# Optimization experiments

Hardware: AMD Instinct MI355X
Metric: run time of the kernel (lower is better)

The kernel has to match this reference:

```python
import jax, jax.numpy as jnp
import numpy as np

B, N, T, H = 64, 15, 256, 128
TEMP = 1.0


def setup_inputs() -> dict:
    key = jax.random.key(0)
    ks = jax.random.split(key, 5)
    node_output = jax.random.normal(ks[0], (B, T, H), jnp.float32)
    neigh_output = jax.random.normal(ks[1], (B, N, T, H), jnp.float32)
    # causal-style mask: True = masked (t' > t); guarantees no fully-masked row
    attn_mask = jnp.broadcast_to(jnp.triu(jnp.ones((T, T), bool), k=1), (B, T, T))
    xav = (2.0 / (H + H)) ** 0.5  # xavier_normal std for square HxH
    Wq = jax.random.normal(ks[2], (H, H), jnp.float32) * xav
    Wk = jax.random.normal(ks[3], (H, H), jnp.float32) * xav
    Wv = jax.random.normal(ks[4], (H, H), jnp.float32) * xav
    z = jnp.zeros((H,), jnp.float32)  # biases init to 0 in init_params
    return dict(node_output=node_output, neigh_output=neigh_output,
                neighbors_number=N, attn_mask=attn_mask,
                Wq=Wq, bq=z, Wk=Wk, bk=z, Wv=Wv, bv=z)


def reference(node_output, neigh_output, neighbors_number, attn_mask,
              Wq, bq, Wk, bk, Wv, bv):
    b, t, h = node_output.shape
    n = neigh_output.shape[1]
    # key/value sequence: self node followed by its n neighbors -> [B, N+1, T, H]
    kv = jnp.concatenate([node_output[:, None], neigh_output], axis=1)
    # Linear (torch convention y = x W^T + b); query repeat collapses to single proj
    q = node_output @ Wq.T + bq                      # [B, T, H]
    k = kv @ Wk.T + bk                               # [B, N+1, T, H]
    v = kv.reshape(b, (n + 1) * t, h) @ Wv.T + bv    # [B, (N+1)*T, H]
    # scores: each query attends separately to every (source, timestep) key
    S = jnp.einsum('bth,bnsh->bnts', q, k)           # [B, N+1, T, T]
    # S_norm computed on the PRE-mask scores (original norms S.data before fill)
    S_norm = jnp.linalg.norm(S.reshape(b, -1), axis=-1)  # [B]
    S = jnp.where(attn_mask[:, None, :, :], -jnp.inf, S)
    S = jnp.transpose(S, (0, 2, 1, 3)) / TEMP        # [B, T, N+1, T]
    # joint softmax over all (N+1)*T keys at once
    A = jax.nn.softmax(S.reshape(b, t, (n + 1) * t), axis=-1)
    out = jnp.einsum('btk,bkh->bth', A, v)           # [B, T, H]
    return out, A.reshape(b, t, n + 1, t), S_norm
```

## Files before the change

kernel.cpp:

```cpp
#include <hip/hip_runtime.h>
#include <math.h>


constexpr int BB   = 64;
constexpr int TT   = 256;
constexpr int HH   = 128;
constexpr int KEYS = 4096;
constexpr int LDK  = 136;
constexpr int LDV  = 72;
constexpr int LDX  = 130;

typedef __attribute__((ext_vector_type(8)))  __bf16 bf16x8;
typedef __attribute__((ext_vector_type(16))) float  f32x16;

union BF8 { unsigned u[4]; bf16x8 v; };

__device__ __forceinline__ float4 ld4(const float* p) {
  return *reinterpret_cast<const float4*>(p);
}
__device__ __forceinline__ unsigned short f2bf(float x) {
  unsigned u = __float_as_uint(x);
  return (unsigned short)((u + 0x7fffu + ((u >> 16) & 1u)) >> 16);
}
__device__ __forceinline__ float bf2f(unsigned short h) {
  return __uint_as_float(((unsigned)h) << 16);
}
__device__ __forceinline__ unsigned packhl(float x) {
  unsigned short hi = f2bf(x);
  unsigned short lo = f2bf(x - bf2f(hi));
  return (unsigned)hi | (((unsigned)lo) << 16);
}
__device__ __forceinline__ void split2(float f0, float f1,
                                       unsigned& hw, unsigned& lw) {
  unsigned short h0 = f2bf(f0), h1 = f2bf(f1);
  unsigned short l0 = f2bf(f0 - bf2f(h0)), l1 = f2bf(f1 - bf2f(h1));
  hw = (unsigned)h0 | (((unsigned)h1) << 16);
  lw = (unsigned)l0 | (((unsigned)l1) << 16);
}
__device__ __forceinline__ void unpack8(const unsigned* p,
                                        bf16x8& hi, bf16x8& lo) {
  uint4 a = *reinterpret_cast<const uint4*>(p);
  uint4 c = *reinterpret_cast<const uint4*>(p + 4);
  BF8 H, L;
  H.u[0] = (a.x & 0xffffu) | (a.y << 16);
  H.u[1] = (a.z & 0xffffu) | (a.w << 16);
  H.u[2] = (c.x & 0xffffu) | (c.y << 16);
  H.u[3] = (c.z & 0xffffu) | (c.w << 16);
  L.u[0] = (a.x >> 16) | (a.y & 0xffff0000u);
  L.u[1] = (a.z >> 16) | (a.w & 0xffff0000u);
  L.u[2] = (c.x >> 16) | (c.y & 0xffff0000u);
  L.u[3] = (c.z >> 16) | (c.w & 0xffff0000u);
  hi = H.v; lo = L.v;
}
__device__ __forceinline__ f32x16 zero16() {
  f32x16 z;
  #pragma unroll
  for (int i = 0; i < 16; ++i) z[i] = 0.f;
  return z;
}
__device__ __forceinline__ f32x16 mfma3(bf16x8 ahi, bf16x8 alo,
                                        bf16x8 bhi, bf16x8 blo, f32x16 c) {
  c = __builtin_amdgcn_mfma_f32_32x32x16_bf16(ahi, bhi, c, 0, 0, 0);
  c = __builtin_amdgcn_mfma_f32_32x32x16_bf16(ahi, blo, c, 0, 0, 0);
  c = __builtin_amdgcn_mfma_f32_32x32x16_bf16(alo, bhi, c, 0, 0, 0);
  return c;
}

template<bool DOV>
__global__ __launch_bounds__(256, 2) void proj_mfma_kernel(
    const float* __restrict__ node, const float* __restrict__ neigh,
    const float* __restrict__ Wk_, const float* __restrict__ bk_,
    const float* __restrict__ Wv_, const float* __restrict__ bv_,
    unsigned* __restrict__ khl, unsigned short* __restrict__ v_t, int mode)
{
  __shared__ unsigned xp[128 * LDX];
  const int tid = threadIdx.x;
  const long r0 = (long)blockIdx.x * 128;

  #pragma unroll
  for (int i = 0; i < 16; ++i) {
    int slot = tid + 256 * i;
    int row = slot >> 5, h0 = (slot & 31) << 2;
    long r = r0 + row;
    const float* src;
    if (mode == 0) {
      src = node + r * HH;
    } else {
      long bb = r >> 12;
      int  n  = (int)((r >> 8) & 15);
      int  t  = (int)(r & 255);
      src = (n == 0) ? (node + (bb * TT + t) * HH)
                     : (neigh + ((bb * 15 + (n - 1)) * (long)TT + t) * HH);
    }
    float4 xv = ld4(src + h0);
    uint4 u;
    u.x = packhl(xv.x); u.y = packhl(xv.y);
    u.z = packhl(xv.z); u.w = packhl(xv.w);
    *reinterpret_cast<uint4*>(&xp[row * LDX + h0]) = u;
  }
  __syncthreads();

  const int l = tid & 63, w = tid >> 6, g = l >> 5, lane31 = l & 31;
  const int j = 32 * w + lane31;

  f32x16 accK[4];
  #pragma unroll
  for (int kt = 0; kt < 4; ++kt) accK[kt] = zero16();
  f32x16 accV[4];
  if constexpr (DOV) {
    #pragma unroll
    for (int kt = 0; kt < 4; ++kt) accV[kt] = zero16();
  }

  #pragma unroll
  for (int hs = 0; hs < 8; ++hs) {
    const int ho = 16 * hs + 8 * g;
    float4 wa = ld4(Wk_ + j * HH + ho), wb = ld4(Wk_ + j * HH + ho + 4);
    BF8 WH, WL;
    split2(wa.x, wa.y, WH.u[0], WL.u[0]);
    split2(wa.z, wa.w, WH.u[1], WL.u[1]);
    split2(wb.x, wb.y, WH.u[2], WL.u[2]);
    split2(wb.z, wb.w, WH.u[3], WL.u[3]);
    bf16x8 xhi[4], xlo[4];
    #pragma unroll
    for (int rt = 0; rt < 4; ++rt)
      unpack8(&xp[(32 * rt + lane31) * LDX + ho], xhi[rt], xlo[rt]);
    #pragma unroll
    for (int rt = 0; rt < 4; ++rt)
      accK[rt] = mfma3(xhi[rt], xlo[rt], WH.v, WL.v, accK[rt]);
    if constexpr (DOV) {
      float4 va = ld4(Wv_ + j * HH + ho), vb = ld4(Wv_ + j * HH + ho + 4);
      BF8 VH, VL;
      split2(va.x, va.y, VH.u[0], VL.u[0]);
      split2(va.z, va.w, VH.u[1], VL.u[1]);
      split2(vb.x, vb.y, VH.u[2], VL.u[2]);
      split2(vb.z, vb.w, VH.u[3], VL.u[3]);
      #pragma unroll
      for (int rt = 0; rt < 4; ++rt)
        accV[rt] = mfma3(VH.v, VL.v, xhi[rt], xlo[rt], accV[rt]);
    }
  }

  const float bK = bk_[j];
  #pragma unroll
  for (int kt = 0; kt < 4; ++kt) {
    #pragma unroll
    for (int reg = 0; reg < 16; ++reg) {
      int rm = (reg & 3) + 8 * (reg >> 2) + 4 * g;
      long r = r0 + 32 * kt + rm;
      khl[r * HH + j] = packhl(accK[kt][reg] + bK);
    }
  }
  if constexpr (DOV) {
    const int bidx = (int)(r0 >> 12);
    const int key0 = (int)(r0 & (KEYS - 1));
    float bvr[16];
    #pragma unroll
    for (int reg = 0; reg < 16; ++reg)
      bvr[reg] = bv_[32 * w + (reg & 3) + 8 * (reg >> 2) + 4 * g];
    #pragma unroll
    for (int kt = 0; kt < 4; ++kt) {
      #pragma unroll
      for (int reg = 0; reg < 16; ++reg) {
        int rm = (reg & 3) + 8 * (reg >> 2) + 4 * g;
        int jrow = 32 * w + rm;
        v_t[((long)(bidx * HH + jrow)) * KEYS + key0 + 32 * kt + lane31] =
            f2bf(accV[kt][reg] + bvr[reg]);
      }
    }
  }
}

__device__ __forceinline__ void load_qfrags(const unsigned* qp, int g,
                                            bf16x8 qhi[8], bf16x8 qlo[8])
{
  #pragma unroll
  for (int hs = 0; hs < 8; ++hs)
    unpack8(qp + 16 * hs + 8 * g, qhi[hs], qlo[hs]);
}

__global__ __launch_bounds__(128, 2) void passA_kernel(
    const unsigned* __restrict__ qhl, const unsigned* __restrict__ khl,
    float* __restrict__ m_part, float* __restrict__ l_part,
    float* __restrict__ ssq_part)
{
  __shared__ unsigned short Khi[64 * LDK];
  __shared__ unsigned short Klo[64 * LDK];
  const int tid = threadIdx.x, l = tid & 63, w = tid >> 6;
  const int g = (l >> 5) & 1, lane31 = l & 31;
  const int bx = blockIdx.x, b = bx >> 4, tq = (bx >> 2) & 3, ks = bx & 3;
  const int t0 = tq * 64;

  bf16x8 qhi[8], qlo[8];
  {
    const int t = t0 + 32 * w + lane31;
    load_qfrags(qhl + ((long)(b * TT + t)) * HH, g, qhi, qlo);
  }

  float mreg[16], lreg[16], ssq = 0.f;
  #pragma unroll
  for (int r = 0; r < 16; ++r) { mreg[r] = -1e30f; lreg[r] = 0.f; }

  for (int kt = 0; kt < 16; ++kt) {
    const int kb = ks * 1024 + kt * 64;
    __syncthreads();
    #pragma unroll
    for (int i = 0; i < 16; ++i) {
      int slot = i * 128 + tid;
      int row = slot >> 5, h0 = (slot & 31) << 2;
      uint4 a = *reinterpret_cast<const uint4*>(
          khl + ((long)(b * KEYS + kb + row)) * HH + h0);
      unsigned h01 = (a.x & 0xffffu) | (a.y << 16);
      unsigned h23 = (a.z & 0xffffu) | (a.w << 16);
      unsigned l01 = (a.x >> 16) | (a.y & 0xffff0000u);
      unsigned l23 = (a.z >> 16) | (a.w & 0xffff0000u);
      *reinterpret_cast<uint2*>(&Khi[row * LDK + h0]) = make_uint2(h01, h23);
      *reinterpret_cast<uint2*>(&Klo[row * LDK + h0]) = make_uint2(l01, l23);
    }
    __syncthreads();

    f32x16 acc0 = zero16(), acc1 = zero16();
    #pragma unroll
    for (int hs = 0; hs < 8; ++hs) {
      const int ho = 16 * hs + 8 * g;
      bf16x8 kh0 = *reinterpret_cast<const bf16x8*>(&Khi[lane31 * LDK + ho]);
      bf16x8 kl0 = *reinterpret_cast<const bf16x8*>(&Klo[lane31 * LDK + ho]);
      bf16x8 kh1 = *reinterpret_cast<const bf16x8*>(&Khi[(32 + lane31) * LDK + ho]);
      bf16x8 kl1 = *reinterpret_cast<const bf16x8*>(&Klo[(32 + lane31) * LDK + ho]);
      acc0 = mfma3(qhi[hs], qlo[hs], kh0, kl0, acc0);
      acc1 = mfma3(qhi[hs], qlo[hs], kh1, kl1, acc1);
    }

    const int st0 = (kb + lane31) & 255;
    const int st1 = (kb + 32 + lane31) & 255;
    #pragma unroll
    for (int reg = 0; reg < 16; ++reg) {
      const int tr = t0 + 32 * w + (reg & 3) + 8 * (reg >> 2) + 4 * g;
      float s0 = acc0[reg], s1 = acc1[reg];
      ssq = fmaf(s0, s0, fmaf(s1, s1, ssq));
      bool msk0 = st0 > tr, msk1 = st1 > tr;
      float v0 = msk0 ? -1e30f : s0;
      float v1 = msk1 ? -1e30f : s1;
      float mn = fmaxf(mreg[reg], fmaxf(v0, v1));
      float sc = __expf(mreg[reg] - mn);
      float p0 = msk0 ? 0.f : __expf(s0 - mn);
      float p1 = msk1 ? 0.f : __expf(s1 - mn);
      lreg[reg] = fmaf(lreg[reg], sc, p0 + p1);
      mreg[reg] = mn;
    }
  }

  #pragma unroll
  for (int reg = 0; reg < 16; ++reg) {
    #pragma unroll
    for (int off = 1; off < 32; off <<= 1) {
      float mo = __shfl_xor(mreg[reg], off);
      float lo = __shfl_xor(lreg[reg], off);
      float mn = fmaxf(mreg[reg], mo);
      lreg[reg] = lreg[reg] * __expf(mreg[reg] - mn) + lo * __expf(mo - mn);
      mreg[reg] = mn;
    }
  }
  if (lane31 == 0) {
    #pragma unroll
    for (int reg = 0; reg < 16; ++reg) {
      const int tr = t0 + 32 * w + (reg & 3) + 8 * (reg >> 2) + 4 * g;
      m_part[ks * (BB * TT) + b * TT + tr] = mreg[reg];
      l_part[ks * (BB * TT) + b * TT + tr] = lreg[reg];
    }
  }
  #pragma unroll
  for (int off = 1; off < 64; off <<= 1) ssq += __shfl_xor(ssq, off);
  __syncthreads();
  float* red = reinterpret_cast<float*>(Khi);
  if (l == 0) red[w] = ssq;
  __syncthreads();
  if (tid == 0) ssq_part[bx] = red[0] + red[1];
}

__global__ void merge_ml_kernel(const float* __restrict__ m_part,
                                const float* __restrict__ l_part,
                                float* __restrict__ m_ws,
                                float* __restrict__ l_ws)
{
  int idx = blockIdx.x * 256 + threadIdx.x;
  if (idx >= BB * TT) return;
  float m = -1e30f;
  #pragma unroll
  for (int k = 0; k < 4; ++k) m = fmaxf(m, m_part[k * (BB * TT) + idx]);
  float lsum = 0.f;
  #pragma unroll
  for (int k = 0; k < 4; ++k)
    lsum += l_part[k * (BB * TT) + idx] * __expf(m_part[k * (BB * TT) + idx] - m);
  m_ws[idx] = m;
  l_ws[idx] = lsum;
}

__global__ __launch_bounds__(256, 2) void passB_kernel(
    const unsigned* __restrict__ qhl, const unsigned* __restrict__ khl,
    const unsigned short* __restrict__ v_t,
    const float* __restrict__ m_ws, const float* __restrict__ l_ws,
    float* __restrict__ A_out, float* __restrict__ opart)
{
  __shared__ unsigned short Khi[64 * LDK];
  __shared__ unsigned short Klo[64 * LDK];
  __shared__ unsigned short Vt[128 * LDV];
  __shared__ unsigned short As[64 * LDV];
  const int tid = threadIdx.x, l = tid & 63, w = tid >> 6;
  const int g = (l >> 5) & 1, lane31 = l & 31;
  const int wt = w & 1, wk = w >> 1;
  const int bx = blockIdx.x, b = bx >> 3, tq = (bx >> 1) & 3, ksb = bx & 1;
  const int t0 = tq * 64;

  bf16x8 qhi[8], qlo[8];
  {
    const int t = t0 + 32 * wt + lane31;
    load_qfrags(qhl + ((long)(b * TT + t)) * HH, g, qhi, qlo);
  }
  float mreg[16], rinv[16];
  #pragma unroll
  for (int reg = 0; reg < 16; ++reg) {
    const int tr = t0 + 32 * wt + (reg & 3) + 8 * (reg >> 2) + 4 * g;
    mreg[reg] = m_ws[b * TT + tr];
    rinv[reg] = 1.0f / l_ws[b * TT + tr];
  }
  f32x16 o0 = zero16(), o1 = zero16();

  for (int kt = 0; kt < 32; ++kt) {
    const int kb = ksb * 2048 + kt * 64;
    __syncthreads();
    #pragma unroll
    for (int i = 0; i < 8; ++i) {
      int slot = i * 256 + tid;
      int row = slot >> 5, h0 = (slot & 31) << 2;
      uint4 a = *reinterpret_cast<const uint4*>(
          khl + ((long)(b * KEYS + kb + row)) * HH + h0);
      unsigned h01 = (a.x & 0xffffu) | (a.y << 16);
      unsigned h23 = (a.z & 0xffffu) | (a.w << 16);
      unsigned l01 = (a.x >> 16) | (a.y & 0xffff0000u);
      unsigned l23 = (a.z >> 16) | (a.w & 0xffff0000u);
      *reinterpret_cast<uint2*>(&Khi[row * LDK + h0]) = make_uint2(h01, h23);
      *reinterpret_cast<uint2*>(&Klo[row * LDK + h0]) = make_uint2(l01, l23);
    }
    #pragma unroll
    for (int i = 0; i < 4; ++i) {
      int slot = i * 256 + tid;
      int hh = slot >> 3, k0 = (slot & 7) << 3;
      uint4 a = *reinterpret_cast<const uint4*>(
          v_t + ((long)(b * HH + hh)) * KEYS + kb + k0);
      *reinterpret_cast<uint4*>(&Vt[hh * LDV + k0]) = a;
    }
    __syncthreads();

    f32x16 acc = zero16();
    #pragma unroll
    for (int hs = 0; hs < 8; ++hs) {
      const int ho = 16 * hs + 8 * g;
      bf16x8 kh = *reinterpret_cast<const bf16x8*>(
          &Khi[(32 * wk + lane31) * LDK + ho]);
      bf16x8 kl = *reinterpret_cast<const bf16x8*>(
          &Klo[(32 * wk + lane31) * LDK + ho]);
      acc = mfma3(qhi[hs], qlo[hs], kh, kl, acc);
    }

    const int key = kb + 32 * wk + lane31;
    const int st = key & 255;
    #pragma unroll
    for (int reg = 0; reg < 16; ++reg) {
      const int rl = 32 * wt + (reg & 3) + 8 * (reg >> 2) + 4 * g;
      const int tr = t0 + rl;
      float a = (st <= tr) ? __expf(acc[reg] - mreg[reg]) * rinv[reg] : 0.f;
      A_out[((long)(b * TT + tr)) * KEYS + key] = a;
      As[rl * LDV + 32 * wk + lane31] = f2bf(a);
    }
    __syncthreads();

    #pragma unroll
    for (int ksx = 0; ksx < 4; ++ksx) {
      const int ko = 16 * ksx + 8 * g;
      bf16x8 af = *reinterpret_cast<const bf16x8*>(
          &As[(32 * wt + lane31) * LDV + ko]);
      bf16x8 v0 = *reinterpret_cast<const bf16x8*>(
          &Vt[(64 * wk + lane31) * LDV + ko]);
      bf16x8 v1 = *reinterpret_cast<const bf16x8*>(
          &Vt[(64 * wk + 32 + lane31) * LDV + ko]);
      o0 = __builtin_amdgcn_mfma_f32_32x32x16_bf16(af, v0, o0, 0, 0, 0);
      o1 = __builtin_amdgcn_mfma_f32_32x32x16_bf16(af, v1, o1, 0, 0, 0);
    }
  }

  #pragma unroll
  for (int reg = 0; reg < 16; ++reg) {
    const int tr = t0 + 32 * wt + (reg & 3) + 8 * (reg >> 2) + 4 * g;
    long base = (long)ksb * (BB * TT * HH) + ((long)(b * TT + tr)) * HH + 64 * wk;
    opart[base + lane31]      = o0[reg];
    opart[base + 32 + lane31] = o1[reg];
  }
}

__global__ void reduce_out_kernel(const float* __restrict__ opart,
                                  float* __restrict__ out)
{
  int i = blockIdx.x * 256 + threadIdx.x;
  const int n4 = BB * TT * HH / 4;
  if (i >= n4) return;
  const float4* p0 = reinterpret_cast<const float4*>(opart);
  const float4* p1 = reinterpret_cast<const float4*>(opart + BB * TT * HH);
  float4 a = p0[i], c = p1[i];
  a.x += c.x; a.y += c.y; a.z += c.z; a.w += c.w;
  *reinterpret_cast<float4*>(out + 4 * (long)i) = a;
}

__global__ void finalize_kernel(const float* __restrict__ ssq_part,
                                float* __restrict__ S_norm)
{
  int b = threadIdx.x;
  if (b < BB) {
    float s = 0.f;
    #pragma unroll
    for (int i = 0; i < 16; ++i) s += ssq_part[b * 16 + i];
    S_norm[b] = sqrtf(s);
  }
}

extern "C" void kernel_launch(void* const* d_in, const int* in_sizes, int n_in,
                              void* d_out, int out_size, void* d_ws, size_t ws_size,
                              hipStream_t stream)
{
  const float* node  = (const float*)d_in[0];
  const float* neigh = (const float*)d_in[1];
  const float* Wq = (const float*)d_in[4];
  const float* bq = (const float*)d_in[5];
  const float* Wk = (const float*)d_in[6];
  const float* bk = (const float*)d_in[7];
  const float* Wv = (const float*)d_in[8];
  const float* bv = (const float*)d_in[9];

  float* out    = (float*)d_out;
  float* A_out  = out + (long)BB * TT * HH;
  float* S_norm = A_out + (long)BB * TT * KEYS;

  unsigned* qhl = (unsigned*)d_ws;
  unsigned* khl = qhl + (long)BB * TT * HH;
  unsigned short* v_t = (unsigned short*)(khl + (long)BB * KEYS * HH);
  float* m_part = (float*)(v_t + (long)BB * HH * KEYS);
  float* l_part = m_part + 4 * BB * TT;
  float* ssq_part = l_part + 4 * BB * TT;
  float* opart = ssq_part + 1024;
  float* m_ws  = opart + 2L * BB * TT * HH;
  float* l_ws  = m_ws + BB * TT;

  proj_mfma_kernel<false><<<dim3(BB * TT / 128), dim3(256), 0, stream>>>(
      node, neigh, Wq, bq, Wq, bq, qhl, v_t, 0);
  proj_mfma_kernel<true><<<dim3(BB * KEYS / 128), dim3(256), 0, stream>>>(
      node, neigh, Wk, bk, Wv, bv, khl, v_t, 1);
  passA_kernel<<<dim3(BB * 16), dim3(128), 0, stream>>>(
      qhl, khl, m_part, l_part, ssq_part);
  merge_ml_kernel<<<dim3((BB * TT + 255) / 256), dim3(256), 0, stream>>>(
      m_part, l_part, m_ws, l_ws);
  passB_kernel<<<dim3(BB * 8), dim3(256), 0, stream>>>(
      qhl, khl, v_t, m_ws, l_ws, A_out, opart);
  reduce_out_kernel<<<dim3((BB * TT * HH / 4 + 255) / 256), dim3(256), 0, stream>>>(
      opart, out);
  finalize_kernel<<<dim3(1), dim3(64), 0, stream>>>(ssq_part, S_norm);
}
```

Baseline: 406.1 us.

## Store Q/K as separate hi/lo bf16 planes, presplit weights, remap blocks per XCD

Q and K projections are now written as two separate bf16 arrays (hi and lo) instead of interleaved hi|lo words. The attention passes can then copy K tiles straight into shared memory with 16-byte loads, and Q fragments no longer need unpacking. A small new kernel splits Wq/Wk/Wv into hi/lo once, so each projection block stops re-splitting fp32 weights. PassA and passB also remap block indices so that blocks sharing a batch and key range land on the same XCD, aiming for better L2 reuse. The cost is an extra kernel launch, a larger workspace, and narrower 2-byte scattered stores in the projection epilogue.

```diff
diff --git a/kernel.cpp b/kernel.cpp
--- a/kernel.cpp
+++ b/kernel.cpp
@@ -8,49 +8,23 @@
 constexpr int KEYS = 4096;
 constexpr int LDK  = 136;
 constexpr int LDV  = 72;
-constexpr int LDX  = 130;
 
 typedef __attribute__((ext_vector_type(8)))  __bf16 bf16x8;
 typedef __attribute__((ext_vector_type(16))) float  f32x16;
-
-union BF8 { unsigned u[4]; bf16x8 v; };
+typedef unsigned short ushort_t;
 
 __device__ __forceinline__ float4 ld4(const float* p) {
   return *reinterpret_cast<const float4*>(p);
 }
-__device__ __forceinline__ unsigned short f2bf(float x) {
-  unsigned u = __float_as_uint(x);
-  return (unsigned short)((u + 0x7fffu + ((u >> 16) & 1u)) >> 16);
-}
-__device__ __forceinline__ float bf2f(unsigned short h) {
+__device__ __forceinline__ ushort_t f2bf(float x) {
+  union { __bf16 b; ushort_t u; } c; c.b = (__bf16)x; return c.u;
+}
+__device__ __forceinline__ float bf2f(ushort_t h) {
   return __uint_as_float(((unsigned)h) << 16);
 }
-__device__ __forceinline__ unsigned packhl(float x) {
-  unsigned short hi = f2bf(x);
-  unsigned short lo = f2bf(x - bf2f(hi));
-  return (unsigned)hi | (((unsigned)lo) << 16);
-}
-__device__ __forceinline__ void split2(float f0, float f1,
-                                       unsigned& hw, unsigned& lw) {
-  unsigned short h0 = f2bf(f0), h1 = f2bf(f1);
-  unsigned short l0 = f2bf(f0 - bf2f(h0)), l1 = f2bf(f1 - bf2f(h1));
-  hw = (unsigned)h0 | (((unsigned)h1) << 16);
-  lw = (unsigned)l0 | (((unsigned)l1) << 16);
-}
-__device__ __forceinline__ void unpack8(const unsigned* p,
-                                        bf16x8& hi, bf16x8& lo) {
-  uint4 a = *reinterpret_cast<const uint4*>(p);
-  uint4 c = *reinterpret_cast<const uint4*>(p + 4);
-  BF8 H, L;
-  H.u[0] = (a.x & 0xffffu) | (a.y << 16);
-  H.u[1] = (a.z & 0xffffu) | (a.w << 16);
-  H.u[2] = (c.x & 0xffffu) | (c.y << 16);
-  H.u[3] = (c.z & 0xffffu) | (c.w << 16);
-  L.u[0] = (a.x >> 16) | (a.y & 0xffff0000u);
-  L.u[1] = (a.z >> 16) | (a.w & 0xffff0000u);
-  L.u[2] = (c.x >> 16) | (c.y & 0xffff0000u);
-  L.u[3] = (c.z >> 16) | (c.w & 0xffff0000u);
-  hi = H.v; lo = L.v;
+__device__ __forceinline__ void splitf(float x, ushort_t& h, ushort_t& l) {
+  h = f2bf(x);
+  l = f2bf(x - bf2f(h));
 }
 __device__ __forceinline__ f32x16 zero16() {
   f32x16 z;
@@ -66,14 +40,33 @@
   return c;
 }
 
+__global__ __launch_bounds__(256) void prep_w_kernel(
+    const float* __restrict__ Wq, const float* __restrict__ Wk,
+    const float* __restrict__ Wv,
+    ushort_t* __restrict__ wqh, ushort_t* __restrict__ wql,
+    ushort_t* __restrict__ wkh, ushort_t* __restrict__ wkl,
+    ushort_t* __restrict__ wvh, ushort_t* __restrict__ wvl)
+{
+  int i = blockIdx.x * 256 + threadIdx.x;
+  if (i >= HH * HH) return;
+  ushort_t h, l;
+  splitf(Wq[i], h, l); wqh[i] = h; wql[i] = l;
+  splitf(Wk[i], h, l); wkh[i] = h; wkl[i] = l;
+  splitf(Wv[i], h, l); wvh[i] = h; wvl[i] = l;
+}
+
 template<bool DOV>
-__global__ __launch_bounds__(256, 2) void proj_mfma_kernel(
+__global__ __launch_bounds__(256, 2) void proj_kernel(
     const float* __restrict__ node, const float* __restrict__ neigh,
-    const float* __restrict__ Wk_, const float* __restrict__ bk_,
-    const float* __restrict__ Wv_, const float* __restrict__ bv_,
-    unsigned* __restrict__ khl, unsigned short* __restrict__ v_t, int mode)
-{
-  __shared__ unsigned xp[128 * LDX];
+    const ushort_t* __restrict__ W1h, const ushort_t* __restrict__ W1l,
+    const float* __restrict__ b1,
+    const ushort_t* __restrict__ WVh, const ushort_t* __restrict__ WVl,
+    const float* __restrict__ bV,
+    ushort_t* __restrict__ yh, ushort_t* __restrict__ yl,
+    ushort_t* __restrict__ v_t, int mode)
+{
+  __shared__ ushort_t xh[128 * LDK];
+  __shared__ ushort_t xl[128 * LDK];
   const int tid = threadIdx.x;
   const long r0 = (long)blockIdx.x * 128;
 
@@ -93,10 +86,15 @@
                      : (neigh + ((bb * 15 + (n - 1)) * (long)TT + t) * HH);
     }
     float4 xv = ld4(src + h0);
-    uint4 u;
-    u.x = packhl(xv.x); u.y = packhl(xv.y);
-    u.z = packhl(xv.z); u.w = packhl(xv.w);
-    *reinterpret_cast<uint4*>(&xp[row * LDX + h0]) = u;
+    ushort_t h0h, h0l, h1h, h1l, h2h, h2l, h3h, h3l;
+    splitf(xv.x, h0h, h0l); splitf(xv.y, h1h, h1l);
+    splitf(xv.z, h2h, h2l); splitf(xv.w, h3h, h3l);
+    *reinterpret_cast<uint2*>(&xh[row * LDK + h0]) =
+        make_uint2((unsigned)h0h | ((unsigned)h1h << 16),
+                   (unsigned)h2h | ((unsigned)h3h << 16));
+    *reinterpret_cast<uint2*>(&xl[row * LDK + h0]) =
+        make_uint2((unsigned)h0l | ((unsigned)h1l << 16),
+                   (unsigned)h2l | ((unsigned)h3l << 16));
   }
   __syncthreads();
 
@@ -115,40 +113,37 @@
   #pragma unroll
   for (int hs = 0; hs < 8; ++hs) {
     const int ho = 16 * hs + 8 * g;
-    float4 wa = ld4(Wk_ + j * HH + ho), wb = ld4(Wk_ + j * HH + ho + 4);
-    BF8 WH, WL;
-    split2(wa.x, wa.y, WH.u[0], WL.u[0]);
-    split2(wa.z, wa.w, WH.u[1], WL.u[1]);
-    split2(wb.x, wb.y, WH.u[2], WL.u[2]);
-    split2(wb.z, wb.w, WH.u[3], WL.u[3]);
-    bf16x8 xhi[4], xlo[4];
+    bf16x8 wh = *reinterpret_cast<const bf16x8*>(W1h + j * HH + ho);
+    bf16x8 wl = *reinterpret_cast<const bf16x8*>(W1l + j * HH + ho);
+    bf16x8 xhf[4], xlf[4];
+    #pragma unroll
+    for (int rt = 0; rt < 4; ++rt) {
+      xhf[rt] = *reinterpret_cast<const bf16x8*>(&xh[(32 * rt + lane31) * LDK + ho]);
+      xlf[rt] = *reinterpret_cast<const bf16x8*>(&xl[(32 * rt + lane31) * LDK + ho]);
+    }
     #pragma unroll
     for (int rt = 0; rt < 4; ++rt)
-      unpack8(&xp[(32 * rt + lane31) * LDX + ho], xhi[rt], xlo[rt]);
-    #pragma unroll
-    for (int rt = 0; rt < 4; ++rt)
-      accK[rt] = mfma3(xhi[rt], xlo[rt], WH.v, WL.v, accK[rt]);
+      accK[rt] = mfma3(xhf[rt], xlf[rt], wh, wl, accK[rt]);
     if constexpr (DOV) {
-      float4 va = ld4(Wv_ + j * HH + ho), vb = ld4(Wv_ + j * HH + ho + 4);
-      BF8 VH, VL;
-      split2(va.x, va.y, VH.u[0], VL.u[0]);
-      split2(va.z, va.w, VH.u[1], VL.u[1]);
-      split2(vb.x, vb.y, VH.u[2], VL.u[2]);
-      split2(vb.z, vb.w, VH.u[3], VL.u[3]);
+      bf16x8 vh = *reinterpret_cast<const bf16x8*>(WVh + j * HH + ho);
+      bf16x8 vl = *reinterpret_cast<const bf16x8*>(WVl + j * HH + ho);
       #pragma unroll
       for (int rt = 0; rt < 4; ++rt)
-        accV[rt] = mfma3(VH.v, VL.v, xhi[rt], xlo[rt], accV[rt]);
-    }
-  }
-
-  const float bK = bk_[j];
+        accV[rt] = mfma3(vh, vl, xhf[rt], xlf[rt], accV[rt]);
+    }
+  }
+
+  const float bK = b1[j];
   #pragma unroll
   for (int kt = 0; kt < 4; ++kt) {
     #pragma unroll
     for (int reg = 0; reg < 16; ++reg) {
       int rm = (reg & 3) + 8 * (reg >> 2) + 4 * g;
       long r = r0 + 32 * kt + rm;
-      khl[r * HH + j] = packhl(accK[kt][reg] + bK);
+      ushort_t h, lo_;
+      splitf(accK[kt][reg] + bK, h, lo_);
+      yh[r * HH + j] = h;
+      yl[r * HH + j] = lo_;
     }
   }
   if constexpr (DOV) {
@@ -157,7 +152,7 @@
     float bvr[16];
     #pragma unroll
     for (int reg = 0; reg < 16; ++reg)
-      bvr[reg] = bv_[32 * w + (reg & 3) + 8 * (reg >> 2) + 4 * g];
+      bvr[reg] = bV[32 * w + (reg & 3) + 8 * (reg >> 2) + 4 * g];
     #pragma unroll
     for (int kt = 0; kt < 4; ++kt) {
       #pragma unroll
@@ -171,30 +166,31 @@
   }
 }
 
-__device__ __forceinline__ void load_qfrags(const unsigned* qp, int g,
-                                            bf16x8 qhi[8], bf16x8 qlo[8])
-{
-  #pragma unroll
-  for (int hs = 0; hs < 8; ++hs)
-    unpack8(qp + 16 * hs + 8 * g, qhi[hs], qlo[hs]);
-}
-
 __global__ __launch_bounds__(128, 2) void passA_kernel(
-    const unsigned* __restrict__ qhl, const unsigned* __restrict__ khl,
+    const ushort_t* __restrict__ q_hi, const ushort_t* __restrict__ q_lo,
+    const ushort_t* __restrict__ k_hi, const ushort_t* __restrict__ k_lo,
     float* __restrict__ m_part, float* __restrict__ l_part,
     float* __restrict__ ssq_part)
 {
-  __shared__ unsigned short Khi[64 * LDK];
-  __shared__ unsigned short Klo[64 * LDK];
+  __shared__ ushort_t Khi[64 * LDK];
+  __shared__ ushort_t Klo[64 * LDK];
   const int tid = threadIdx.x, l = tid & 63, w = tid >> 6;
   const int g = (l >> 5) & 1, lane31 = l & 31;
-  const int bx = blockIdx.x, b = bx >> 4, tq = (bx >> 2) & 3, ks = bx & 3;
+  const int p = blockIdx.x;
+  const int xcd = p & 7, slot = p >> 3;
+  const int pair = xcd * 32 + (slot >> 2);
+  const int tq = slot & 3;
+  const int b = pair >> 2, ks = pair & 3;
   const int t0 = tq * 64;
 
   bf16x8 qhi[8], qlo[8];
   {
-    const int t = t0 + 32 * w + lane31;
-    load_qfrags(qhl + ((long)(b * TT + t)) * HH, g, qhi, qlo);
+    const long qb = ((long)(b * TT + t0 + 32 * w + lane31)) * HH;
+    #pragma unroll
+    for (int hs = 0; hs < 8; ++hs) {
+      qhi[hs] = *reinterpret_cast<const bf16x8*>(q_hi + qb + 16 * hs + 8 * g);
+      qlo[hs] = *reinterpret_cast<const bf16x8*>(q_lo + qb + 16 * hs + 8 * g);
+    }
   }
 
   float mreg[16], lreg[16], ssq = 0.f;
@@ -205,17 +201,14 @@
     const int kb = ks * 1024 + kt * 64;
     __syncthreads();
     #pragma unroll
-    for (int i = 0; i < 16; ++i) {
-      int slot = i * 128 + tid;
-      int row = slot >> 5, h0 = (slot & 31) << 2;
-      uint4 a = *reinterpret_cast<const uint4*>(
-          khl + ((long)(b * KEYS + kb + row)) * HH + h0);
-      unsigned h01 = (a.x & 0xffffu) | (a.y << 16);
-      unsigned h23 = (a.z & 0xffffu) | (a.w << 16);
-      unsigned l01 = (a.x >> 16) | (a.y & 0xffff0000u);
-      unsigned l23 = (a.z >> 16) | (a.w & 0xffff0000u);
-      *reinterpret_cast<uint2*>(&Khi[row * LDK + h0]) = make_uint2(h01, h23);
-      *reinterpret_cast<uint2*>(&Klo[row * LDK + h0]) = make_uint2(l01, l23);
+    for (int i = 0; i < 8; ++i) {
+      int slot2 = i * 128 + tid;
+      int row = slot2 >> 4, c0 = (slot2 & 15) << 3;
+      const long gsrc = ((long)(b * KEYS + kb + row)) * HH + c0;
+      *reinterpret_cast<uint4*>(&Khi[row * LDK + c0]) =
+          *reinterpret_cast<const uint4*>(k_hi + gsrc);
+      *reinterpret_cast<uint4*>(&Klo[row * LDK + c0]) =
+          *reinterpret_cast<const uint4*>(k_lo + gsrc);
     }
     __syncthreads();
 
@@ -275,7 +268,7 @@
   float* red = reinterpret_cast<float*>(Khi);
   if (l == 0) red[w] = ssq;
   __syncthreads();
-  if (tid == 0) ssq_part[bx] = red[0] + red[1];
+  if (tid == 0) ssq_part[b * 16 + tq * 4 + ks] = red[0] + red[1];
 }
 
 __global__ void merge_ml_kernel(const float* __restrict__ m_part,
@@ -297,25 +290,34 @@
 }
 
 __global__ __launch_bounds__(256, 2) void passB_kernel(
-    const unsigned* __restrict__ qhl, const unsigned* __restrict__ khl,
-    const unsigned short* __restrict__ v_t,
+    const ushort_t* __restrict__ q_hi, const ushort_t* __restrict__ q_lo,
+    const ushort_t* __restrict__ k_hi, const ushort_t* __restrict__ k_lo,
+    const ushort_t* __restrict__ v_t,
     const float* __restrict__ m_ws, const float* __restrict__ l_ws,
     float* __restrict__ A_out, float* __restrict__ opart)
 {
-  __shared__ unsigned short Khi[64 * LDK];
-  __shared__ unsigned short Klo[64 * LDK];
-  __shared__ unsigned short Vt[128 * LDV];
-  __shared__ unsigned short As[64 * LDV];
+  __shared__ ushort_t Khi[64 * LDK];
+  __shared__ ushort_t Klo[64 * LDK];
+  __shared__ ushort_t Vt[128 * LDV];
+  __shared__ ushort_t As[64 * LDV];
   const int tid = threadIdx.x, l = tid & 63, w = tid >> 6;
   const int g = (l >> 5) & 1, lane31 = l & 31;
   const int wt = w & 1, wk = w >> 1;
-  const int bx = blockIdx.x, b = bx >> 3, tq = (bx >> 1) & 3, ksb = bx & 1;
+  const int p = blockIdx.x;
+  const int xcd = p & 7, slot = p >> 3;
+  const int pair = xcd * 16 + (slot >> 2);
+  const int tq = slot & 3;
+  const int b = pair >> 1, ksb = pair & 1;
   const int t0 = tq * 64;
 
   bf16x8 qhi[8], qlo[8];
   {
-    const int t = t0 + 32 * wt + lane31;
-    load_qfrags(qhl + ((long)(b * TT + t)) * HH, g, qhi, qlo);
+    const long qb = ((long)(b * TT + t0 + 32 * wt + lane31)) * HH;
+    #pragma unroll
+    for (int hs = 0; hs < 8; ++hs) {
+      qhi[hs] = *reinterpret_cast<const bf16x8*>(q_hi + qb + 16 * hs + 8 * g);
+      qlo[hs] = *reinterpret_cast<const bf16x8*>(q_lo + qb + 16 * hs + 8 * g);
+    }
   }
   float mreg[16], rinv[16];
   #pragma unroll
@@ -330,25 +332,22 @@
     const int kb = ksb * 2048 + kt * 64;
     __syncthreads();
     #pragma unroll
-    for (int i = 0; i < 8; ++i) {
-      int slot = i * 256 + tid;
-      int row = slot >> 5, h0 = (slot & 31) << 2;
-      uint4 a = *reinterpret_cast<const uint4*>(
-          khl + ((long)(b * KEYS + kb + row)) * HH + h0);
-      unsigned h01 = (a.x & 0xffffu) | (a.y << 16);
-      unsigned h23 = (a.z & 0xffffu) | (a.w << 16);
-      unsigned l01 = (a.x >> 16) | (a.y & 0xffff0000u);
-      unsigned l23 = (a.z >> 16) | (a.w & 0xffff0000u);
-      *reinterpret_cast<uint2*>(&Khi[row * LDK + h0]) = make_uint2(h01, h23);
-      *reinterpret_cast<uint2*>(&Klo[row * LDK + h0]) = make_uint2(l01, l23);
-    }
-    #pragma unroll
     for (int i = 0; i < 4; ++i) {
-      int slot = i * 256 + tid;
-      int hh = slot >> 3, k0 = (slot & 7) << 3;
-      uint4 a = *reinterpret_cast<const uint4*>(
-          v_t + ((long)(b * HH + hh)) * KEYS + kb + k0);
-      *reinterpret_cast<uint4*>(&Vt[hh * LDV + k0]) = a;
+      int slot2 = i * 256 + tid;
+      int row = slot2 >> 4, c0 = (slot2 & 15) << 3;
+      const long gsrc = ((long)(b * KEYS + kb + row)) * HH + c0;
+      *reinterpret_cast<uint4*>(&Khi[row * LDK + c0]) =
+          *reinterpret_cast<const uint4*>(k_hi + gsrc);
+      *reinterpret_cast<uint4*>(&Klo[row * LDK + c0]) =
+          *reinterpret_cast<const uint4*>(k_lo + gsrc);
+    }
+    #pragma unroll
+    for (int i = 0; i < 4; ++i) {
+      int slot2 = i * 256 + tid;
+      int hh = slot2 >> 3, k0 = (slot2 & 7) << 3;
+      *reinterpret_cast<uint4*>(&Vt[hh * LDV + k0]) =
+          *reinterpret_cast<const uint4*>(
+              v_t + ((long)(b * HH + hh)) * KEYS + kb + k0);
     }
     __syncthreads();
 
@@ -440,26 +439,36 @@
   float* A_out  = out + (long)BB * TT * HH;
   float* S_norm = A_out + (long)BB * TT * KEYS;
 
-  unsigned* qhl = (unsigned*)d_ws;
-  unsigned* khl = qhl + (long)BB * TT * HH;
-  unsigned short* v_t = (unsigned short*)(khl + (long)BB * KEYS * HH);
-  float* m_part = (float*)(v_t + (long)BB * HH * KEYS);
+  ushort_t* q_hi = (ushort_t*)d_ws;
+  ushort_t* q_lo = q_hi + (long)BB * TT * HH;
+  ushort_t* k_hi = q_lo + (long)BB * TT * HH;
+  ushort_t* k_lo = k_hi + (long)BB * KEYS * HH;
+  ushort_t* v_t  = k_lo + (long)BB * KEYS * HH;
+  ushort_t* wqh  = v_t + (long)BB * HH * KEYS;
+  ushort_t* wql  = wqh + HH * HH;
+  ushort_t* wkh  = wql + HH * HH;
+  ushort_t* wkl  = wkh + HH * HH;
+  ushort_t* wvh  = wkl + HH * HH;
+  ushort_t* wvl  = wvh + HH * HH;
+  float* m_part = (float*)(wvl + HH * HH);
   float* l_part = m_part + 4 * BB * TT;
   float* ssq_part = l_part + 4 * BB * TT;
   float* opart = ssq_part + 1024;
   float* m_ws  = opart + 2L * BB * TT * HH;
   float* l_ws  = m_ws + BB * TT;
 
-  proj_mfma_kernel<false><<<dim3(BB * TT / 128), dim3(256), 0, stream>>>(
-      node, neigh, Wq, bq, Wq, bq, qhl, v_t, 0);
-  proj_mfma_kernel<true><<<dim3(BB * KEYS / 128), dim3(256), 0, stream>>>(
-      node, neigh, Wk, bk, Wv, bv, khl, v_t, 1);
+  prep_w_kernel<<<dim3((HH * HH + 255) / 256), dim3(256), 0, stream>>>(
+      Wq, Wk, Wv, wqh, wql, wkh, wkl, wvh, wvl);
+  proj_kernel<false><<<dim3(BB * TT / 128), dim3(256), 0, stream>>>(
+      node, neigh, wqh, wql, bq, wvh, wvl, bv, q_hi, q_lo, v_t, 0);
+  proj_kernel<true><<<dim3(BB * KEYS / 128), dim3(256), 0, stream>>>(
+      node, neigh, wkh, wkl, bk, wvh, wvl, bv, k_hi, k_lo, v_t, 1);
   passA_kernel<<<dim3(BB * 16), dim3(128), 0, stream>>>(
-      qhl, khl, m_part, l_part, ssq_part);
+      q_hi, q_lo, k_hi, k_lo, m_part, l_part, ssq_part);
   merge_ml_kernel<<<dim3((BB * TT + 255) / 256), dim3(256), 0, stream>>>(
       m_part, l_part, m_ws, l_ws);
   passB_kernel<<<dim3(BB * 8), dim3(256), 0, stream>>>(
-      qhl, khl, v_t, m_ws, l_ws, A_out, opart);
+      q_hi, q_lo, k_hi, k_lo, v_t, m_ws, l_ws, A_out, opart);
   reduce_out_kernel<<<dim3((BB * TT * HH / 4 + 255) / 256), dim3(256), 0, stream>>>(
       opart, out);
   finalize_kernel<<<dim3(1), dim3(64), 0, stream>>>(ssq_part, S_norm);
```

Measured after the change: 385.0 us. 1.05x faster.
